# Optimization experiments

Measured on AMD Instinct MI355X. Metric: run time of the kernel, lower is better.

## Reference

```python
import jax, jax.numpy as jnp
import numpy as np

N = 50000      # nodes
E = 800000     # edges
F = 128        # node feature dim (= output_size, residual)
H = 128        # hidden_size

def _uniform_fan_avg(key, shape):
    # VarianceScaling(scale=1.0, mode='fan_avg', distribution='uniform')
    fan_avg = (shape[0] + shape[1]) / 2.0
    limit = np.sqrt(3.0 / fan_avg)
    return jax.random.uniform(key, shape, jnp.float32, -limit, limit)

def setup_inputs() -> dict:
    key = jax.random.key(0)
    ks = jax.random.split(key, 16)
    h = jax.random.normal(ks[0], (N, F), jnp.float32)
    pos = jax.random.normal(ks[1], (N, 3), jnp.float32)
    senders = jax.random.randint(ks[2], (E,), 0, N, jnp.int32)
    receivers = jax.random.randint(ks[3], (E,), 0, N, jnp.int32)
    # edge_mlp: Linear(2F+1 -> H) silu, Linear(H -> H) silu (activate_final=True)
    eW1 = _uniform_fan_avg(ks[4], (2 * F + 1, H)); eb1 = jnp.zeros((H,), jnp.float32)
    eW2 = _uniform_fan_avg(ks[5], (H, H)); eb2 = jnp.zeros((H,), jnp.float32)
    # node_mlp: Linear(F+H -> H) silu, Linear(H -> F) (no final act)
    nW1 = _uniform_fan_avg(ks[6], (F + H, H)); nb1 = jnp.zeros((H,), jnp.float32)
    nW2 = _uniform_fan_avg(ks[7], (H, F)); nb2 = jnp.zeros((F,), jnp.float32)
    # pos_correction_mlp: Linear(H -> H) silu, Linear(H -> 1, no bias, UniformScaling(dt))
    pW1 = _uniform_fan_avg(ks[8], (H, H)); pb1 = jnp.zeros((H,), jnp.float32)
    dt = 0.001
    pW2 = jax.random.uniform(ks[9], (H, 1), jnp.float32, -dt, dt) * np.sqrt(3.0)
    return {"h": h, "pos": pos, "senders": senders, "receivers": receivers,
            "eW1": eW1, "eb1": eb1, "eW2": eW2, "eb2": eb2,
            "nW1": nW1, "nb1": nb1, "nW2": nW2, "nb2": nb2,
            "pW1": pW1, "pb1": pb1, "pW2": pW2}

def reference(h, pos, senders, receivers,
              eW1, eb1, eW2, eb2,
              nW1, nb1, nW2, nb2,
              pW1, pb1, pW2):
    n = h.shape[0]
    # _coord2radial (normalize=False)
    coord_diff = pos[senders] - pos[receivers]            # [E,3]
    radial = jnp.sum(coord_diff ** 2, axis=1, keepdims=True)  # [E,1]
    # edge update (_message): concat(h[senders], h[receivers], radial) -> edge_mlp
    msg_in = jnp.concatenate([h[senders], h[receivers], radial], axis=-1)  # [E,2F+1]
    msg = jax.nn.silu(msg_in @ eW1 + eb1)
    msg = jax.nn.silu(msg @ eW2 + eb2)                    # [E,H]
    # node update (_update): aggregate messages at receivers, node_mlp, residual
    agg = jax.ops.segment_sum(msg, receivers, num_segments=n)  # [N,H]
    x = jnp.concatenate([h, agg], axis=-1)                # [N,F+H]
    x = jax.nn.silu(x @ nW1 + nb1)
    x = x @ nW2 + nb2                                     # [N,F]
    h_new = h + x                                         # residual
    # position update (_pos_update)
    pc = jax.nn.silu(msg @ pW1 + pb1) @ pW2               # [E,1]
    trans = jnp.clip(coord_diff * pc, -100, 100)          # [E,3]
    pos_new = pos + jax.ops.segment_sum(trans, senders, num_segments=n)
    return h_new, pos_new
```

## Files before the change

### kernel.cpp

```cpp
#include <hip/hip_runtime.h>
#include <hip/hip_bf16.h>

#define NNODES 50000
#define NEDGES 800000
#define EB 1024
#define SCAN_BLOCKS 196
#define TRN_BLOCKS 448

typedef short bf16x8 __attribute__((ext_vector_type(8)));
typedef float f32x4 __attribute__((ext_vector_type(4)));
typedef unsigned short u16;
typedef unsigned int u32;

__device__ __forceinline__ u16 f2bf(float f) {
    __hip_bfloat16 b = __float2bfloat16(f);
    return *reinterpret_cast<u16*>(&b);
}
__device__ __forceinline__ float bf2f(u16 v) {
    u32 u = ((u32)v) << 16;
    return __uint_as_float(u);
}
__device__ __forceinline__ u32 pack2(float a, float b) {
    __hip_bfloat162 t = __float22bfloat162_rn(float2{a, b});
    return *reinterpret_cast<u32*>(&t);
}
__device__ __forceinline__ float fast_silu(float x) {
    float e = __builtin_amdgcn_exp2f(-1.442695040888963f * x);
    return x * __builtin_amdgcn_rcpf(1.0f + e);
}
__device__ __forceinline__ bf16x8 ld8(const u16* p) {
    return *(const bf16x8*)p;
}
__device__ __forceinline__ f32x4 mfma16(bf16x8 a, bf16x8 b, f32x4 c) {
    return __builtin_amdgcn_mfma_f32_16x16x32_bf16(a, b, c, 0, 0, 0);
}
__device__ __forceinline__ void bar_lds() {
    asm volatile("s_waitcnt lgkmcnt(0)\n\ts_barrier" ::: "memory");
}

__global__ void prep_kernel(const float* __restrict__ eW1, const float* __restrict__ eW2,
                            const float* __restrict__ pW1, const float* __restrict__ nW1,
                            const float* __restrict__ nW2,
                            u16* __restrict__ eW1T, u16* __restrict__ eW2T,
                            u16* __restrict__ pW1T, u16* __restrict__ nW1T,
                            u16* __restrict__ nW2T,
                            const int* __restrict__ rcv, int* __restrict__ counts) {
    int b = blockIdx.x;
    if (b < TRN_BLOCKS) {
        int i = b * 256 + threadIdx.x;
        const float* src; u16* dst; int K;
        if (i < 32768)      { src = eW1; dst = eW1T; K = 256; }
        else if (i < 49152) { src = eW2; dst = eW2T; K = 128; i -= 32768; }
        else if (i < 65536) { src = pW1; dst = pW1T; K = 128; i -= 49152; }
        else if (i < 98304) { src = nW1; dst = nW1T; K = 256; i -= 65536; }
        else                { src = nW2; dst = nW2T; K = 128; i -= 98304; }
        int n = i / K, k = i - n * K;
        dst[i] = f2bf(src[k * 128 + n]);
    } else {
        int e = (b - TRN_BLOCKS) * 256 + threadIdx.x;
        if (e < NEDGES) atomicAdd(&counts[rcv[e]], 1);
    }
}

__global__ __launch_bounds__(256) void gemm_p(
    const float* __restrict__ h, const u16* __restrict__ eW1T,
    const u16* __restrict__ nW1T, const float* __restrict__ eb1,
    u16* __restrict__ P)
{
    const int tid  = threadIdx.x;
    const int w    = tid >> 6;
    const int lane = tid & 63;
    const int m    = lane & 15;
    const int quad = lane >> 4;
    const int ksub = quad * 8;

    bf16x8 bw[4][6];
    float bias[6];
    #pragma unroll
    for (int cc = 0; cc < 6; cc++) {
        int C = 96 * w + 16 * cc + m;
        const u16* bp;
        if (C < 128)      { bp = eW1T + C * 256;               bias[cc] = 0.5f * eb1[C]; }
        else if (C < 256) { bp = eW1T + (C - 128) * 256 + 128; bias[cc] = 0.5f * eb1[C - 128]; }
        else              { bp = nW1T + (C - 256) * 256;       bias[cc] = 0.f; }
        #pragma unroll
        for (int t = 0; t < 4; t++) bw[t][cc] = ld8(bp + t * 32 + ksub);
    }
    const int base = blockIdx.x * 64;
    #pragma unroll
    for (int mt = 0; mt < 4; mt++) {
        int nm = base + mt * 16 + m;
        if (nm >= NNODES) nm = NNODES - 1;
        bf16x8 afr[4];
        #pragma unroll
        for (int t = 0; t < 4; t++) {
            const float* ap = h + (size_t)nm * 128 + t * 32 + ksub;
            f32x4 lo = *(const f32x4*)ap;
            f32x4 hi = *(const f32x4*)(ap + 4);
            #pragma unroll
            for (int j = 0; j < 4; j++) {
                afr[t][j]     = (short)f2bf(lo[j]);
                afr[t][4 + j] = (short)f2bf(hi[j]);
            }
        }
        f32x4 acc[6];
        #pragma unroll
        for (int cc = 0; cc < 6; cc++) acc[cc] = (f32x4){0,0,0,0};
        #pragma unroll
        for (int t = 0; t < 4; t++)
            #pragma unroll
            for (int cc = 0; cc < 6; cc++)
                acc[cc] = mfma16(afr[t], bw[t][cc], acc[cc]);
        #pragma unroll
        for (int cc = 0; cc < 6; cc++) {
            int C = 96 * w + 16 * cc + m;
            #pragma unroll
            for (int r = 0; r < 4; r++) {
                int nr = base + mt * 16 + quad * 4 + r;
                if (nr < NNODES) P[(size_t)nr * 384 + C] = f2bf(acc[cc][r] + bias[cc]);
            }
        }
    }
}

__global__ void scan1(const int* __restrict__ counts, int* __restrict__ excl,
                      int* __restrict__ blkSum) {
    __shared__ int tmp[256];
    int tx = threadIdx.x;
    int i = blockIdx.x * 256 + tx;
    int v = (i < NNODES) ? counts[i] : 0;
    tmp[tx] = v;
    __syncthreads();
    for (int off = 1; off < 256; off <<= 1) {
        int t = (tx >= off) ? tmp[tx - off] : 0;
        __syncthreads();
        tmp[tx] += t;
        __syncthreads();
    }
    if (i < NNODES) excl[i] = tmp[tx] - v;
    if (tx == 255) blkSum[blockIdx.x] = tmp[255];
}
__global__ void scan2(const int* __restrict__ blkSum, int* __restrict__ blkOff) {
    __shared__ int tmp[256];
    int tx = threadIdx.x;
    int v = (tx < SCAN_BLOCKS) ? blkSum[tx] : 0;
    tmp[tx] = v;
    __syncthreads();
    for (int off = 1; off < 256; off <<= 1) {
        int t = (tx >= off) ? tmp[tx - off] : 0;
        __syncthreads();
        tmp[tx] += t;
        __syncthreads();
    }
    if (tx < SCAN_BLOCKS) blkOff[tx] = tmp[tx] - v;
}
__global__ void scan3(const int* __restrict__ excl, const int* __restrict__ blkOff,
                      int* __restrict__ cursor) {
    int i = blockIdx.x * 256 + threadIdx.x;
    if (i < NNODES) cursor[i] = excl[i] + blkOff[blockIdx.x];
}
__global__ void scatter_kernel(const int* __restrict__ rcv, int* __restrict__ cursor,
                               int* __restrict__ perm) {
    int e = blockIdx.x * 256 + threadIdx.x;
    if (e < NEDGES) {
        int p = atomicAdd(&cursor[rcv[e]], 1);
        perm[p] = e;
    }
}

struct __align__(16) EdgeLds {
    u16   m1[64 * 136];
    u16   msg[64 * 136];
    float diff[64][4];
    float pcpart[4][64];
    float wlast[128];
    int   sndloc[64];
    int   rcvloc[64];
    unsigned long long bmap;
};

__global__ __launch_bounds__(256, 4) void edge_kernel(
    const u16* __restrict__ P, const float* __restrict__ pos,
    const int* __restrict__ snd, const int* __restrict__ rcv,
    const int* __restrict__ perm,
    const float* __restrict__ eW1last,
    const u16* __restrict__ eW2T, const float* __restrict__ eb2,
    const u16* __restrict__ pW1T, const float* __restrict__ pb1,
    const float* __restrict__ pW2,
    float* __restrict__ agg, float* __restrict__ posacc)
{
    __shared__ EdgeLds S;
    const int tid  = threadIdx.x;
    const int w    = tid >> 6;
    const int lane = tid & 63;
    const int m    = lane & 15;
    const int quad = lane >> 4;
    const int ksub = quad * 8;

    bf16x8 bw2[4][2], bp1[4][2];
    float b2v[2], pb1v[2], pw2v[2];
    #pragma unroll
    for (int cc = 0; cc < 2; cc++) {
        int col = (2 * w + cc) * 16 + m;
        #pragma unroll
        for (int t = 0; t < 4; t++) {
            bw2[t][cc] = ld8(eW2T + col * 128 + t * 32 + ksub);
            bp1[t][cc] = ld8(pW1T + col * 128 + t * 32 + ksub);
        }
        b2v[cc]  = eb2[col];
        pb1v[cc] = pb1[col];
        pw2v[cc] = pW2[col];
    }
    if (tid < 128) S.wlast[tid] = eW1last[tid];

    const int NT  = NEDGES / 64;
    const int xcd = blockIdx.x & 7;
    const int ib  = blockIdx.x >> 3;
    const int per = (NT + 7) / 8;
    const int t0  = xcd * per;
    const int t1  = (t0 + per < NT) ? t0 + per : NT;

    int eg_n = 0, s_n = 0, r_n = 0;
    if (t0 + ib < t1) {
        eg_n = perm[(t0 + ib) * 64 + lane];
        s_n = snd[eg_n]; r_n = rcv[eg_n];
    }

    for (int t = t0 + ib; t < t1; t += 128) {
        const int s = s_n, r = r_n;
        const int tn = t + 128;
        const int tp = (tn < t1) ? tn : t;
        int eg2 = perm[tp * 64 + lane];

        float d0 = pos[s * 3 + 0] - pos[r * 3 + 0];
        float d1 = pos[s * 3 + 1] - pos[r * 3 + 1];
        float d2 = pos[s * 3 + 2] - pos[r * 3 + 2];
        float rad = d0 * d0 + d1 * d1 + d2 * d2;

        bar_lds();
        if (tid < 64) {
            S.sndloc[tid] = s; S.rcvloc[tid] = r;
            S.diff[tid][0] = d0; S.diff[tid][1] = d1; S.diff[tid][2] = d2;
            int pv = __shfl_up(r, 1);
            unsigned long long bm = __ballot(lane > 0 && r != pv);
            if (tid == 0) S.bmap = bm;
        }
        {
            const int sw = lane >> 3;
            const u16* pa = P + (size_t)s * 384 + w * 32;
            const u16* pb = P + (size_t)r * 384 + 128 + w * 32;
            #pragma unroll
            for (int k = 0; k < 4; k++) {
                bf16x8 va = ld8(pa + k * 8);
                bf16x8 vb = ld8(pb + k * 8);
                u32 pk[4];
                #pragma unroll
                for (int jj = 0; jj < 4; jj++) {
                    int col = w * 32 + k * 8 + jj * 2;
                    float2 wl = *(const float2*)&S.wlast[col];
                    float v0 = bf2f((u16)va[jj * 2])     + bf2f((u16)vb[jj * 2])     + rad * wl.x;
                    float v1 = bf2f((u16)va[jj * 2 + 1]) + bf2f((u16)vb[jj * 2 + 1]) + rad * wl.y;
                    pk[jj] = pack2(fast_silu(v0), fast_silu(v1));
                }
                int chunk = (w * 4 + k) ^ sw;
                *(uint4*)&S.m1[lane * 136 + chunk * 8] =
                    make_uint4(pk[0], pk[1], pk[2], pk[3]);
            }
        }
        s_n = snd[eg2]; r_n = rcv[eg2]; eg_n = eg2;

        bar_lds();
        #pragma unroll
        for (int mt = 0; mt < 4; mt++) {
            const int rs = mt * 2 + (m >> 3);
            const int row = mt * 16 + m;
            f32x4 acc0 = (f32x4){0,0,0,0}, acc1 = (f32x4){0,0,0,0};
            #pragma unroll
            for (int t4 = 0; t4 < 4; t4++) {
                bf16x8 a = *(const bf16x8*)&S.m1[row * 136 + ((t4 * 4 + quad) ^ rs) * 8];
                acc0 = mfma16(a, bw2[t4][0], acc0);
                acc1 = mfma16(a, bw2[t4][1], acc1);
            }
            #pragma unroll
            for (int cc = 0; cc < 2; cc++) {
                f32x4 acc = cc ? acc1 : acc0;
                int col = (2 * w + cc) * 16 + m;
                #pragma unroll
                for (int rr = 0; rr < 4; rr++) {
                    int orow = mt * 16 + quad * 4 + rr;
                    S.msg[orow * 136 + col] = f2bf(fast_silu(acc[rr] + b2v[cc]));
                }
            }
        }
        bar_lds();
        #pragma unroll
        for (int mt = 0; mt < 4; mt++) {
            f32x4 acc0 = (f32x4){0,0,0,0}, acc1 = (f32x4){0,0,0,0};
            #pragma unroll
            for (int t4 = 0; t4 < 4; t4++) {
                bf16x8 a = *(const bf16x8*)&S.msg[(mt * 16 + m) * 136 + t4 * 32 + ksub];
                acc0 = mfma16(a, bp1[t4][0], acc0);
                acc1 = mfma16(a, bp1[t4][1], acc1);
            }
            float p4[4];
            #pragma unroll
            for (int rr = 0; rr < 4; rr++)
                p4[rr] = fast_silu(acc0[rr] + pb1v[0]) * pw2v[0]
                       + fast_silu(acc1[rr] + pb1v[1]) * pw2v[1];
            #pragma unroll
            for (int mask = 1; mask < 16; mask <<= 1) {
                #pragma unroll
                for (int rr = 0; rr < 4; rr++) p4[rr] += __shfl_xor(p4[rr], mask);
            }
            if (m == 0) {
                #pragma unroll
                for (int rr = 0; rr < 4; rr++)
                    S.pcpart[w][mt * 16 + quad * 4 + rr] = p4[rr];
            }
        }
        {
            int half = tid >> 7, col = tid & 127;
            int r0 = half * 32;
            u32 bm32 = __builtin_amdgcn_readfirstlane((u32)(S.bmap >> r0)) & ~1u;
            float a = 0.f;
            int cur = S.rcvloc[r0];
            int rr = r0;
            const int end0 = r0 + 32;
            while (true) {
                int nb = bm32 ? (r0 + __builtin_ctz(bm32)) : end0;
                for (; rr < nb; ++rr) a += bf2f(S.msg[rr * 136 + col]);
                atomicAdd(&agg[(size_t)cur * 128 + col], a);
                if (nb == end0) break;
                a = 0.f;
                cur = S.rcvloc[nb];
                bm32 &= bm32 - 1;
            }
        }
        bar_lds();
        if (tid < 192) {
            int ee = tid / 3, c = tid - ee * 3;
            float pc = S.pcpart[0][ee] + S.pcpart[1][ee] + S.pcpart[2][ee] + S.pcpart[3][ee];
            float tr = S.diff[ee][c] * pc;
            tr = fminf(fmaxf(tr, -100.f), 100.f);
            atomicAdd(&posacc[S.sndloc[ee] * 3 + c], tr);
        }
    }
}

__global__ __launch_bounds__(256, 4) void node_kernel(
    const u16* __restrict__ P, const float* __restrict__ h,
    const float* __restrict__ agg,
    const u16* __restrict__ nW1T, const float* __restrict__ nb1,
    const u16* __restrict__ nW2T, const float* __restrict__ nb2,
    const float* __restrict__ pos, const float* __restrict__ posacc,
    float* __restrict__ out)
{
    __shared__ alignas(16) u16 m1[64 * 136];
    const int tid  = threadIdx.x;
    const int w    = tid >> 6;
    const int lane = tid & 63;
    const int m    = lane & 15;
    const int quad = lane >> 4;
    const int ksub = quad * 8;

    bf16x8 bw1[4][2], bw2[4][2];
    float b1v[2], b2v[2];
    #pragma unroll
    for (int cc = 0; cc < 2; cc++) {
        int col = (2 * w + cc) * 16 + m;
        #pragma unroll
        for (int t = 0; t < 4; t++) {
            bw1[t][cc] = ld8(nW1T + col * 256 + 128 + t * 32 + ksub);
            bw2[t][cc] = ld8(nW2T + col * 128 + t * 32 + ksub);
        }
        b1v[cc] = nb1[col];
        b2v[cc] = nb2[col];
    }
    const int base = blockIdx.x * 64;
    #pragma unroll
    for (int mt = 0; mt < 4; mt++) {
        int nm = base + mt * 16 + m;
        if (nm >= NNODES) nm = NNODES - 1;
        f32x4 acc0 = (f32x4){0,0,0,0}, acc1 = (f32x4){0,0,0,0};
        #pragma unroll
        for (int t = 0; t < 4; t++) {
            const float* ap = agg + (size_t)nm * 128 + t * 32 + ksub;
            f32x4 lo = *(const f32x4*)ap;
            f32x4 hi = *(const f32x4*)(ap + 4);
            bf16x8 a;
            #pragma unroll
            for (int j = 0; j < 4; j++) {
                a[j]     = (short)f2bf(lo[j]);
                a[4 + j] = (short)f2bf(hi[j]);
            }
            acc0 = mfma16(a, bw1[t][0], acc0);
            acc1 = mfma16(a, bw1[t][1], acc1);
        }
        #pragma unroll
        for (int cc = 0; cc < 2; cc++) {
            f32x4 acc = cc ? acc1 : acc0;
            int col = (2 * w + cc) * 16 + m;
            #pragma unroll
            for (int rr = 0; rr < 4; rr++) {
                int row = mt * 16 + quad * 4 + rr;
                int nrc = base + row; if (nrc >= NNODES) nrc = NNODES - 1;
                float v = acc[rr] + bf2f(P[(size_t)nrc * 384 + 256 + col]) + b1v[cc];
                m1[row * 136 + col] = f2bf(fast_silu(v));
            }
        }
    }
    __syncthreads();
    #pragma unroll
    for (int mt = 0; mt < 4; mt++) {
        f32x4 acc0 = (f32x4){0,0,0,0}, acc1 = (f32x4){0,0,0,0};
        #pragma unroll
        for (int t = 0; t < 4; t++) {
            bf16x8 a = *(const bf16x8*)&m1[(mt * 16 + m) * 136 + t * 32 + ksub];
            acc0 = mfma16(a, bw2[t][0], acc0);
            acc1 = mfma16(a, bw2[t][1], acc1);
        }
        #pragma unroll
        for (int cc = 0; cc < 2; cc++) {
            f32x4 acc = cc ? acc1 : acc0;
            int col = (2 * w + cc) * 16 + m;
            #pragma unroll
            for (int rr = 0; rr < 4; rr++) {
                int nr = base + mt * 16 + quad * 4 + rr;
                if (nr < NNODES)
                    out[(size_t)nr * 128 + col] = acc[rr] + b2v[cc] + h[(size_t)nr * 128 + col];
            }
        }
    }
    if (tid < 192) {
        int i = blockIdx.x * 192 + tid;
        if (i < NNODES * 3) out[NNODES * 128 + i] = pos[i] + posacc[i];
    }
}

extern "C" void kernel_launch(void* const* d_in, const int* in_sizes, int n_in,
                              void* d_out, int out_size, void* d_ws, size_t ws_size,
                              hipStream_t stream) {
    (void)in_sizes; (void)n_in; (void)out_size; (void)ws_size;
    const float* h   = (const float*)d_in[0];
    const float* pos = (const float*)d_in[1];
    const int*   snd = (const int*)d_in[2];
    const int*   rcv = (const int*)d_in[3];
    const float* eW1 = (const float*)d_in[4];
    const float* eb1 = (const float*)d_in[5];
    const float* eW2 = (const float*)d_in[6];
    const float* eb2 = (const float*)d_in[7];
    const float* nW1 = (const float*)d_in[8];
    const float* nb1 = (const float*)d_in[9];
    const float* nW2 = (const float*)d_in[10];
    const float* nb2 = (const float*)d_in[11];
    const float* pW1 = (const float*)d_in[12];
    const float* pb1 = (const float*)d_in[13];
    const float* pW2 = (const float*)d_in[14];
    float* out = (float*)d_out;

    float* agg    = (float*)d_ws;
    float* posacc = agg + (size_t)NNODES * 128;
    u16* P    = (u16*)(posacc + (size_t)NNODES * 3);
    u16* eW1T = P + (size_t)NNODES * 384;
    u16* eW2T = eW1T + 128 * 256;
    u16* pW1T = eW2T + 128 * 128;
    u16* nW1T = pW1T + 128 * 128;
    u16* nW2T = nW1T + 128 * 256;
    int* counts = (int*)(nW2T + 128 * 128);
    int* excl   = counts + 50048;
    int* blkSum = excl + 50048;
    int* blkOff = blkSum + 256;
    int* cursor = blkOff + 256;
    int* perm   = cursor + 50048;

    hipMemsetAsync(agg, 0, (size_t)NNODES * 131 * sizeof(float), stream);
    hipMemsetAsync(counts, 0, 50048 * sizeof(int), stream);

    prep_kernel<<<TRN_BLOCKS + (NEDGES + 255) / 256, 256, 0, stream>>>(
        eW1, eW2, pW1, nW1, nW2, eW1T, eW2T, pW1T, nW1T, nW2T, rcv, counts);

    gemm_p<<<(NNODES + 63) / 64, 256, 0, stream>>>(h, eW1T, nW1T, eb1, P);

    scan1<<<SCAN_BLOCKS, 256, 0, stream>>>(counts, excl, blkSum);
    scan2<<<1, 256, 0, stream>>>(blkSum, blkOff);
    scan3<<<SCAN_BLOCKS, 256, 0, stream>>>(excl, blkOff, cursor);
    scatter_kernel<<<(NEDGES + 255) / 256, 256, 0, stream>>>(rcv, cursor, perm);

    edge_kernel<<<EB, 256, 0, stream>>>(
        P, pos, snd, rcv, perm,
        eW1 + 256 * 128,
        eW2T, eb2, pW1T, pb1, pW2,
        agg, posacc);

    node_kernel<<<(NNODES + 63) / 64, 256, 0, stream>>>(
        P, h, agg, nW1T, nb1, nW2T, nb2, pos, posacc, out);
}
```

Baseline: 454.9 us.

## Prefetch sender rows into LDS asynchronously and fold scan3 into scatter

The edge kernel now uses global_load_lds to stage the next tile's sender projection rows straight into LDS while the current tile's MFMA work runs. It ping-pongs two LDS buffers, so the buffer that held the message tile also receives the prefetch. Separately, the scan3 kernel is dropped: scatter computes each slot as excl+blkOff plus an atomic delta counter, which saves a launch but adds two loads per edge. The risk is a race or mismatched staging layout, since the prefetch into bufM is issued while other waves may still be reading bufM in the pc stage.

```diff
diff --git a/kernel.cpp b/kernel.cpp
--- a/kernel.cpp
+++ b/kernel.cpp
@@ -36,6 +36,11 @@
 }
 __device__ __forceinline__ void bar_lds() {
     asm volatile("s_waitcnt lgkmcnt(0)\n\ts_barrier" ::: "memory");
+}
+__device__ __forceinline__ void stage16(const u16* g, u16* l) {
+    __builtin_amdgcn_global_load_lds(
+        (const __attribute__((address_space(1))) u32*)(const void*)g,
+        (__attribute__((address_space(3))) u32*)(void*)l, 16, 0, 0);
 }
 
 __global__ void prep_kernel(const float* __restrict__ eW1, const float* __restrict__ eW2,
@@ -154,23 +159,20 @@
     }
     if (tx < SCAN_BLOCKS) blkOff[tx] = tmp[tx] - v;
 }
-__global__ void scan3(const int* __restrict__ excl, const int* __restrict__ blkOff,
-                      int* __restrict__ cursor) {
-    int i = blockIdx.x * 256 + threadIdx.x;
-    if (i < NNODES) cursor[i] = excl[i] + blkOff[blockIdx.x];
-}
-__global__ void scatter_kernel(const int* __restrict__ rcv, int* __restrict__ cursor,
+__global__ void scatter_kernel(const int* __restrict__ rcv, const int* __restrict__ excl,
+                               const int* __restrict__ blkOff, int* __restrict__ delta,
                                int* __restrict__ perm) {
     int e = blockIdx.x * 256 + threadIdx.x;
     if (e < NEDGES) {
-        int p = atomicAdd(&cursor[rcv[e]], 1);
+        int r = rcv[e];
+        int p = excl[r] + blkOff[r >> 8] + atomicAdd(&delta[r], 1);
         perm[p] = e;
     }
 }
 
 struct __align__(16) EdgeLds {
-    u16   m1[64 * 136];
-    u16   msg[64 * 136];
+    u16   b0[64 * 136];
+    u16   b1[64 * 136];
     float diff[64][4];
     float pcpart[4][64];
     float wlast[128];
@@ -220,10 +222,16 @@
     const int t0  = xcd * per;
     const int t1  = (t0 + per < NT) ? t0 + per : NT;
 
-    int eg_n = 0, s_n = 0, r_n = 0;
+    u16* bufS = S.b0;
+    u16* bufM = S.b1;
+
+    int s_n = 0, r_n = 0;
     if (t0 + ib < t1) {
-        eg_n = perm[(t0 + ib) * 64 + lane];
-        s_n = snd[eg_n]; r_n = rcv[eg_n];
+        int eg = perm[(t0 + ib) * 64 + lane];
+        s_n = snd[eg]; r_n = rcv[eg];
+        #pragma unroll
+        for (int k = 0; k < 4; k++)
+            stage16(P + (size_t)s_n * 384 + w * 32 + k * 8, bufS + w * 2048 + k * 512);
     }
 
     for (int t = t0 + ib; t < t1; t += 128) {
@@ -247,27 +255,30 @@
         }
         {
             const int sw = lane >> 3;
-            const u16* pa = P + (size_t)s * 384 + w * 32;
-            const u16* pb = P + (size_t)r * 384 + 128 + w * 32;
+            asm volatile("s_waitcnt vmcnt(0)" ::: "memory");
+            bf16x8 va[4];
+            #pragma unroll
+            for (int k = 0; k < 4; k++)
+                va[k] = *(const bf16x8*)&bufS[w * 2048 + k * 512 + lane * 8];
+            const u16* pbp = P + (size_t)r * 384 + 128 + w * 32;
             #pragma unroll
             for (int k = 0; k < 4; k++) {
-                bf16x8 va = ld8(pa + k * 8);
-                bf16x8 vb = ld8(pb + k * 8);
+                bf16x8 vb = ld8(pbp + k * 8);
                 u32 pk[4];
                 #pragma unroll
                 for (int jj = 0; jj < 4; jj++) {
                     int col = w * 32 + k * 8 + jj * 2;
                     float2 wl = *(const float2*)&S.wlast[col];
-                    float v0 = bf2f((u16)va[jj * 2])     + bf2f((u16)vb[jj * 2])     + rad * wl.x;
-                    float v1 = bf2f((u16)va[jj * 2 + 1]) + bf2f((u16)vb[jj * 2 + 1]) + rad * wl.y;
+                    float v0 = bf2f((u16)va[k][jj * 2])     + bf2f((u16)vb[jj * 2])     + rad * wl.x;
+                    float v1 = bf2f((u16)va[k][jj * 2 + 1]) + bf2f((u16)vb[jj * 2 + 1]) + rad * wl.y;
                     pk[jj] = pack2(fast_silu(v0), fast_silu(v1));
                 }
                 int chunk = (w * 4 + k) ^ sw;
-                *(uint4*)&S.m1[lane * 136 + chunk * 8] =
+                *(uint4*)&bufM[lane * 136 + chunk * 8] =
                     make_uint4(pk[0], pk[1], pk[2], pk[3]);
             }
         }
-        s_n = snd[eg2]; r_n = rcv[eg2]; eg_n = eg2;
+        s_n = snd[eg2]; r_n = rcv[eg2];
 
         bar_lds();
         #pragma unroll
@@ -277,7 +288,7 @@
             f32x4 acc0 = (f32x4){0,0,0,0}, acc1 = (f32x4){0,0,0,0};
             #pragma unroll
             for (int t4 = 0; t4 < 4; t4++) {
-                bf16x8 a = *(const bf16x8*)&S.m1[row * 136 + ((t4 * 4 + quad) ^ rs) * 8];
+                bf16x8 a = *(const bf16x8*)&bufM[row * 136 + ((t4 * 4 + quad) ^ rs) * 8];
                 acc0 = mfma16(a, bw2[t4][0], acc0);
                 acc1 = mfma16(a, bw2[t4][1], acc1);
             }
@@ -288,17 +299,21 @@
                 #pragma unroll
                 for (int rr = 0; rr < 4; rr++) {
                     int orow = mt * 16 + quad * 4 + rr;
-                    S.msg[orow * 136 + col] = f2bf(fast_silu(acc[rr] + b2v[cc]));
+                    bufS[orow * 136 + col] = f2bf(fast_silu(acc[rr] + b2v[cc]));
                 }
             }
         }
         bar_lds();
+        #pragma unroll
+        for (int k = 0; k < 4; k++)
+            stage16(P + (size_t)s_n * 384 + w * 32 + k * 8, bufM + w * 2048 + k * 512);
+
         #pragma unroll
         for (int mt = 0; mt < 4; mt++) {
             f32x4 acc0 = (f32x4){0,0,0,0}, acc1 = (f32x4){0,0,0,0};
             #pragma unroll
             for (int t4 = 0; t4 < 4; t4++) {
-                bf16x8 a = *(const bf16x8*)&S.msg[(mt * 16 + m) * 136 + t4 * 32 + ksub];
+                bf16x8 a = *(const bf16x8*)&bufS[(mt * 16 + m) * 136 + t4 * 32 + ksub];
                 acc0 = mfma16(a, bp1[t4][0], acc0);
                 acc1 = mfma16(a, bp1[t4][1], acc1);
             }
@@ -328,7 +343,7 @@
             const int end0 = r0 + 32;
             while (true) {
                 int nb = bm32 ? (r0 + __builtin_ctz(bm32)) : end0;
-                for (; rr < nb; ++rr) a += bf2f(S.msg[rr * 136 + col]);
+                for (; rr < nb; ++rr) a += bf2f(bufS[rr * 136 + col]);
                 atomicAdd(&agg[(size_t)cur * 128 + col], a);
                 if (nb == end0) break;
                 a = 0.f;
@@ -344,6 +359,7 @@
             tr = fminf(fmaxf(tr, -100.f), 100.f);
             atomicAdd(&posacc[S.sndloc[ee] * 3 + c], tr);
         }
+        u16* tmpb = bufS; bufS = bufM; bufM = tmpb;
     }
 }
 
@@ -467,14 +483,14 @@
     u16* nW1T = pW1T + 128 * 128;
     u16* nW2T = nW1T + 128 * 256;
     int* counts = (int*)(nW2T + 128 * 128);
-    int* excl   = counts + 50048;
+    int* delta  = counts + 50048;
+    int* excl   = delta + 50048;
     int* blkSum = excl + 50048;
     int* blkOff = blkSum + 256;
-    int* cursor = blkOff + 256;
-    int* perm   = cursor + 50048;
+    int* perm   = blkOff + 256;
 
     hipMemsetAsync(agg, 0, (size_t)NNODES * 131 * sizeof(float), stream);
-    hipMemsetAsync(counts, 0, 50048 * sizeof(int), stream);
+    hipMemsetAsync(counts, 0, 2 * 50048 * sizeof(int), stream);
 
     prep_kernel<<<TRN_BLOCKS + (NEDGES + 255) / 256, 256, 0, stream>>>(
         eW1, eW2, pW1, nW1, nW2, eW1T, eW2T, pW1T, nW1T, nW2T, rcv, counts);
@@ -483,8 +499,7 @@
 
     scan1<<<SCAN_BLOCKS, 256, 0, stream>>>(counts, excl, blkSum);
     scan2<<<1, 256, 0, stream>>>(blkSum, blkOff);
-    scan3<<<SCAN_BLOCKS, 256, 0, stream>>>(excl, blkOff, cursor);
-    scatter_kernel<<<(NEDGES + 255) / 256, 256, 0, stream>>>(rcv, cursor, perm);
+    scatter_kernel<<<(NEDGES + 255) / 256, 256, 0, stream>>>(rcv, excl, blkOff, delta, perm);
 
     edge_kernel<<<EB, 256, 0, stream>>>(
         P, pos, snd, rcv, perm,
```

New measurement: 504.2 us. +10.8%, slower.

## Precompute sorted sender/receiver pairs and coord diffs during scatter; swizzle msg LDS

Applied to the files above, without the earlier changes.

The scatter kernel now drops the separate scan3 pass and computes each edge's slot directly from excl, blkOff and a per-node atomic delta. It writes sender/receiver pairs and coordinate differences plus the squared radius into receiver-sorted arrays. The edge kernel then reads these contiguously instead of chasing the perm indirection and gathering pos per edge, and it issues the sender-row P loads before the barrier. The msg LDS tile gets an XOR swizzle to avoid bank conflicts, and the segment-sum uses 128 threads each reading two columns at once. The cost is more scatter work and extra workspace for the 24-byte-per-edge arrays.

```diff
diff --git a/kernel.cpp b/kernel.cpp
--- a/kernel.cpp
+++ b/kernel.cpp
@@ -154,17 +154,21 @@
     }
     if (tx < SCAN_BLOCKS) blkOff[tx] = tmp[tx] - v;
 }
-__global__ void scan3(const int* __restrict__ excl, const int* __restrict__ blkOff,
-                      int* __restrict__ cursor) {
-    int i = blockIdx.x * 256 + threadIdx.x;
-    if (i < NNODES) cursor[i] = excl[i] + blkOff[blockIdx.x];
-}
-__global__ void scatter_kernel(const int* __restrict__ rcv, int* __restrict__ cursor,
-                               int* __restrict__ perm) {
+__global__ void scatter_kernel(const int* __restrict__ rcv, const int* __restrict__ snd,
+                               const float* __restrict__ pos,
+                               const int* __restrict__ excl, const int* __restrict__ blkOff,
+                               int* __restrict__ delta,
+                               int2* __restrict__ sr, float4* __restrict__ d4) {
     int e = blockIdx.x * 256 + threadIdx.x;
     if (e < NEDGES) {
-        int p = atomicAdd(&cursor[rcv[e]], 1);
-        perm[p] = e;
+        int r = rcv[e];
+        int s = snd[e];
+        int p = excl[r] + blkOff[r >> 8] + atomicAdd(&delta[r], 1);
+        float d0 = pos[s * 3 + 0] - pos[r * 3 + 0];
+        float d1 = pos[s * 3 + 1] - pos[r * 3 + 1];
+        float d2 = pos[s * 3 + 2] - pos[r * 3 + 2];
+        sr[p] = make_int2(s, r);
+        d4[p] = make_float4(d0, d1, d2, d0 * d0 + d1 * d1 + d2 * d2);
     }
 }
 
@@ -180,9 +184,8 @@
 };
 
 __global__ __launch_bounds__(256, 4) void edge_kernel(
-    const u16* __restrict__ P, const float* __restrict__ pos,
-    const int* __restrict__ snd, const int* __restrict__ rcv,
-    const int* __restrict__ perm,
+    const u16* __restrict__ P,
+    const int2* __restrict__ sr, const float4* __restrict__ d4,
     const float* __restrict__ eW1last,
     const u16* __restrict__ eW2T, const float* __restrict__ eb2,
     const u16* __restrict__ pW1T, const float* __restrict__ pb1,
@@ -220,46 +223,45 @@
     const int t0  = xcd * per;
     const int t1  = (t0 + per < NT) ? t0 + per : NT;
 
-    int eg_n = 0, s_n = 0, r_n = 0;
-    if (t0 + ib < t1) {
-        eg_n = perm[(t0 + ib) * 64 + lane];
-        s_n = snd[eg_n]; r_n = rcv[eg_n];
-    }
+    int2 srn = make_int2(0, 0);
+    if (t0 + ib < t1) srn = sr[(size_t)(t0 + ib) * 64 + lane];
 
     for (int t = t0 + ib; t < t1; t += 128) {
-        const int s = s_n, r = r_n;
+        const int s = srn.x, r = srn.y;
         const int tn = t + 128;
         const int tp = (tn < t1) ? tn : t;
-        int eg2 = perm[tp * 64 + lane];
-
-        float d0 = pos[s * 3 + 0] - pos[r * 3 + 0];
-        float d1 = pos[s * 3 + 1] - pos[r * 3 + 1];
-        float d2 = pos[s * 3 + 2] - pos[r * 3 + 2];
-        float rad = d0 * d0 + d1 * d1 + d2 * d2;
+
+        int2 sr2  = sr[(size_t)tp * 64 + lane];
+        float4 dd = d4[(size_t)t * 64 + lane];
+        const u16* pap = P + (size_t)s * 384 + w * 32;
+        bf16x8 va0 = ld8(pap);
+        bf16x8 va1 = ld8(pap + 8);
+        bf16x8 va2 = ld8(pap + 16);
+        bf16x8 va3 = ld8(pap + 24);
 
         bar_lds();
         if (tid < 64) {
             S.sndloc[tid] = s; S.rcvloc[tid] = r;
-            S.diff[tid][0] = d0; S.diff[tid][1] = d1; S.diff[tid][2] = d2;
+            *(float4*)&S.diff[tid][0] = dd;
             int pv = __shfl_up(r, 1);
             unsigned long long bm = __ballot(lane > 0 && r != pv);
             if (tid == 0) S.bmap = bm;
         }
         {
+            const float rad = dd.w;
             const int sw = lane >> 3;
-            const u16* pa = P + (size_t)s * 384 + w * 32;
-            const u16* pb = P + (size_t)r * 384 + 128 + w * 32;
+            const u16* pbp = P + (size_t)r * 384 + 128 + w * 32;
+            bf16x8 va[4] = {va0, va1, va2, va3};
             #pragma unroll
             for (int k = 0; k < 4; k++) {
-                bf16x8 va = ld8(pa + k * 8);
-                bf16x8 vb = ld8(pb + k * 8);
+                bf16x8 vb = ld8(pbp + k * 8);
                 u32 pk[4];
                 #pragma unroll
                 for (int jj = 0; jj < 4; jj++) {
                     int col = w * 32 + k * 8 + jj * 2;
                     float2 wl = *(const float2*)&S.wlast[col];
-                    float v0 = bf2f((u16)va[jj * 2])     + bf2f((u16)vb[jj * 2])     + rad * wl.x;
-                    float v1 = bf2f((u16)va[jj * 2 + 1]) + bf2f((u16)vb[jj * 2 + 1]) + rad * wl.y;
+                    float v0 = bf2f((u16)va[k][jj * 2])     + bf2f((u16)vb[jj * 2])     + rad * wl.x;
+                    float v1 = bf2f((u16)va[k][jj * 2 + 1]) + bf2f((u16)vb[jj * 2 + 1]) + rad * wl.y;
                     pk[jj] = pack2(fast_silu(v0), fast_silu(v1));
                 }
                 int chunk = (w * 4 + k) ^ sw;
@@ -267,7 +269,7 @@
                     make_uint4(pk[0], pk[1], pk[2], pk[3]);
             }
         }
-        s_n = snd[eg2]; r_n = rcv[eg2]; eg_n = eg2;
+        srn = sr2;
 
         bar_lds();
         #pragma unroll
@@ -285,20 +287,24 @@
             for (int cc = 0; cc < 2; cc++) {
                 f32x4 acc = cc ? acc1 : acc0;
                 int col = (2 * w + cc) * 16 + m;
+                int CC = col >> 3, cl = col & 7;
                 #pragma unroll
                 for (int rr = 0; rr < 4; rr++) {
                     int orow = mt * 16 + quad * 4 + rr;
-                    S.msg[orow * 136 + col] = f2bf(fast_silu(acc[rr] + b2v[cc]));
+                    S.msg[orow * 136 + ((CC ^ (orow >> 3)) << 3) + cl] =
+                        f2bf(fast_silu(acc[rr] + b2v[cc]));
                 }
             }
         }
         bar_lds();
         #pragma unroll
         for (int mt = 0; mt < 4; mt++) {
+            const int row = mt * 16 + m;
+            const int rs = mt * 2 + (m >> 3);
             f32x4 acc0 = (f32x4){0,0,0,0}, acc1 = (f32x4){0,0,0,0};
             #pragma unroll
             for (int t4 = 0; t4 < 4; t4++) {
-                bf16x8 a = *(const bf16x8*)&S.msg[(mt * 16 + m) * 136 + t4 * 32 + ksub];
+                bf16x8 a = *(const bf16x8*)&S.msg[row * 136 + (((t4 * 4 + quad) ^ rs)) * 8];
                 acc0 = mfma16(a, bp1[t4][0], acc0);
                 acc1 = mfma16(a, bp1[t4][1], acc1);
             }
@@ -318,20 +324,28 @@
                     S.pcpart[w][mt * 16 + quad * 4 + rr] = p4[rr];
             }
         }
-        {
-            int half = tid >> 7, col = tid & 127;
+        if (tid < 128) {
+            int half = tid >> 6, cp = tid & 63;
+            int c0 = cp * 2;
             int r0 = half * 32;
             u32 bm32 = __builtin_amdgcn_readfirstlane((u32)(S.bmap >> r0)) & ~1u;
-            float a = 0.f;
+            float a0 = 0.f, a1 = 0.f;
             int cur = S.rcvloc[r0];
             int rr = r0;
             const int end0 = r0 + 32;
+            const int chunkbase = (cp >> 2) ;
+            const int off = (cp & 3) * 2;
             while (true) {
                 int nb = bm32 ? (r0 + __builtin_ctz(bm32)) : end0;
-                for (; rr < nb; ++rr) a += bf2f(S.msg[rr * 136 + col]);
-                atomicAdd(&agg[(size_t)cur * 128 + col], a);
+                for (; rr < nb; ++rr) {
+                    u32 v = *(const u32*)&S.msg[rr * 136 + ((chunkbase ^ (rr >> 3)) << 3) + off];
+                    a0 += bf2f((u16)(v & 0xffff));
+                    a1 += bf2f((u16)(v >> 16));
+                }
+                atomicAdd(&agg[(size_t)cur * 128 + c0], a0);
+                atomicAdd(&agg[(size_t)cur * 128 + c0 + 1], a1);
                 if (nb == end0) break;
-                a = 0.f;
+                a0 = 0.f; a1 = 0.f;
                 cur = S.rcvloc[nb];
                 bm32 &= bm32 - 1;
             }
@@ -467,14 +481,15 @@
     u16* nW1T = pW1T + 128 * 128;
     u16* nW2T = nW1T + 128 * 256;
     int* counts = (int*)(nW2T + 128 * 128);
-    int* excl   = counts + 50048;
+    int* delta  = counts + 50048;
+    int* excl   = delta + 50048;
     int* blkSum = excl + 50048;
     int* blkOff = blkSum + 256;
-    int* cursor = blkOff + 256;
-    int* perm   = cursor + 50048;
+    int2*   sr  = (int2*)(blkOff + 256);
+    float4* d4  = (float4*)(sr + NEDGES);
 
     hipMemsetAsync(agg, 0, (size_t)NNODES * 131 * sizeof(float), stream);
-    hipMemsetAsync(counts, 0, 50048 * sizeof(int), stream);
+    hipMemsetAsync(counts, 0, 2 * 50048 * sizeof(int), stream);
 
     prep_kernel<<<TRN_BLOCKS + (NEDGES + 255) / 256, 256, 0, stream>>>(
         eW1, eW2, pW1, nW1, nW2, eW1T, eW2T, pW1T, nW1T, nW2T, rcv, counts);
@@ -483,11 +498,11 @@
 
     scan1<<<SCAN_BLOCKS, 256, 0, stream>>>(counts, excl, blkSum);
     scan2<<<1, 256, 0, stream>>>(blkSum, blkOff);
-    scan3<<<SCAN_BLOCKS, 256, 0, stream>>>(excl, blkOff, cursor);
-    scatter_kernel<<<(NEDGES + 255) / 256, 256, 0, stream>>>(rcv, cursor, perm);
+    scatter_kernel<<<(NEDGES + 255) / 256, 256, 0, stream>>>(
+        rcv, snd, pos, excl, blkOff, delta, sr, d4);
 
     edge_kernel<<<EB, 256, 0, stream>>>(
-        P, pos, snd, rcv, perm,
+        P, sr, d4,
         eW1 + 256 * 128,
         eW2T, eb2, pW1T, pb1, pW2,
         agg, posacc);
```

Measured after the change: 536.2 us. +17.9%, slower.

## Fold scan3 into scatter, drop edge-kernel barrier, restructure agg segment reduction

Applied to the files above, without the earlier changes.

Removes the scan3 kernel: scatter now computes each slot as the exclusive prefix plus block offset plus an atomic per-node delta. The delta array is zeroed by the same memset as counts. In the edge kernel, each wave's partial position-correction sum now goes straight into the clipped position atomics. This drops the pcpart LDS buffer and the final barrier, but issues four times as many posacc atomics and clips per-wave partial sums instead of the full sum. The message segment reduction now has each wave cover 16 rows with two columns per thread, and the wlast weights are read as vector loads.

```diff
diff --git a/kernel.cpp b/kernel.cpp
--- a/kernel.cpp
+++ b/kernel.cpp
@@ -154,16 +154,13 @@
     }
     if (tx < SCAN_BLOCKS) blkOff[tx] = tmp[tx] - v;
 }
-__global__ void scan3(const int* __restrict__ excl, const int* __restrict__ blkOff,
-                      int* __restrict__ cursor) {
-    int i = blockIdx.x * 256 + threadIdx.x;
-    if (i < NNODES) cursor[i] = excl[i] + blkOff[blockIdx.x];
-}
-__global__ void scatter_kernel(const int* __restrict__ rcv, int* __restrict__ cursor,
+__global__ void scatter_kernel(const int* __restrict__ rcv, const int* __restrict__ excl,
+                               const int* __restrict__ blkOff, int* __restrict__ delta,
                                int* __restrict__ perm) {
     int e = blockIdx.x * 256 + threadIdx.x;
     if (e < NEDGES) {
-        int p = atomicAdd(&cursor[rcv[e]], 1);
+        int r = rcv[e];
+        int p = excl[r] + blkOff[r >> 8] + atomicAdd(&delta[r], 1);
         perm[p] = e;
     }
 }
@@ -172,7 +169,6 @@
     u16   m1[64 * 136];
     u16   msg[64 * 136];
     float diff[64][4];
-    float pcpart[4][64];
     float wlast[128];
     int   sndloc[64];
     int   rcvloc[64];
@@ -240,26 +236,29 @@
         bar_lds();
         if (tid < 64) {
             S.sndloc[tid] = s; S.rcvloc[tid] = r;
-            S.diff[tid][0] = d0; S.diff[tid][1] = d1; S.diff[tid][2] = d2;
+            S.diff[tid][0] = d0; S.diff[tid][1] = d1;
+            S.diff[tid][2] = d2; S.diff[tid][3] = 0.f;
             int pv = __shfl_up(r, 1);
             unsigned long long bm = __ballot(lane > 0 && r != pv);
             if (tid == 0) S.bmap = bm;
         }
         {
             const int sw = lane >> 3;
-            const u16* pa = P + (size_t)s * 384 + w * 32;
-            const u16* pb = P + (size_t)r * 384 + 128 + w * 32;
+            const u16* pap = P + (size_t)s * 384 + w * 32;
+            const u16* pbp = P + (size_t)r * 384 + 128 + w * 32;
             #pragma unroll
             for (int k = 0; k < 4; k++) {
-                bf16x8 va = ld8(pa + k * 8);
-                bf16x8 vb = ld8(pb + k * 8);
+                bf16x8 va = ld8(pap + k * 8);
+                bf16x8 vb = ld8(pbp + k * 8);
+                f32x4 wla = *(const f32x4*)&S.wlast[w * 32 + k * 8];
+                f32x4 wlb = *(const f32x4*)&S.wlast[w * 32 + k * 8 + 4];
                 u32 pk[4];
                 #pragma unroll
                 for (int jj = 0; jj < 4; jj++) {
-                    int col = w * 32 + k * 8 + jj * 2;
-                    float2 wl = *(const float2*)&S.wlast[col];
-                    float v0 = bf2f((u16)va[jj * 2])     + bf2f((u16)vb[jj * 2])     + rad * wl.x;
-                    float v1 = bf2f((u16)va[jj * 2 + 1]) + bf2f((u16)vb[jj * 2 + 1]) + rad * wl.y;
+                    float wx = (jj < 2) ? wla[jj * 2]     : wlb[(jj - 2) * 2];
+                    float wy = (jj < 2) ? wla[jj * 2 + 1] : wlb[(jj - 2) * 2 + 1];
+                    float v0 = bf2f((u16)va[jj * 2])     + bf2f((u16)vb[jj * 2])     + rad * wx;
+                    float v1 = bf2f((u16)va[jj * 2 + 1]) + bf2f((u16)vb[jj * 2 + 1]) + rad * wy;
                     pk[jj] = pack2(fast_silu(v0), fast_silu(v1));
                 }
                 int chunk = (w * 4 + k) ^ sw;
@@ -314,35 +313,43 @@
             }
             if (m == 0) {
                 #pragma unroll
-                for (int rr = 0; rr < 4; rr++)
-                    S.pcpart[w][mt * 16 + quad * 4 + rr] = p4[rr];
+                for (int rr = 0; rr < 4; rr++) {
+                    int row = mt * 16 + quad * 4 + rr;
+                    float pc = p4[rr];
+                    f32x4 dd = *(const f32x4*)&S.diff[row][0];
+                    int sl = S.sndloc[row];
+                    float tr0 = fminf(fmaxf(dd[0] * pc, -100.f), 100.f);
+                    float tr1 = fminf(fmaxf(dd[1] * pc, -100.f), 100.f);
+                    float tr2 = fminf(fmaxf(dd[2] * pc, -100.f), 100.f);
+                    atomicAdd(&posacc[sl * 3 + 0], tr0);
+                    atomicAdd(&posacc[sl * 3 + 1], tr1);
+                    atomicAdd(&posacc[sl * 3 + 2], tr2);
+                }
             }
         }
         {
-            int half = tid >> 7, col = tid & 127;
-            int r0 = half * 32;
-            u32 bm32 = __builtin_amdgcn_readfirstlane((u32)(S.bmap >> r0)) & ~1u;
-            float a = 0.f;
+            int cp = tid & 63;
+            int c0 = cp * 2;
+            int r0 = w * 16;
+            u32 bm = __builtin_amdgcn_readfirstlane(((u32)(S.bmap >> r0)) & 0xFFFFu) & ~1u;
+            float a0 = 0.f, a1 = 0.f;
             int cur = S.rcvloc[r0];
             int rr = r0;
-            const int end0 = r0 + 32;
+            const int end0 = r0 + 16;
             while (true) {
-                int nb = bm32 ? (r0 + __builtin_ctz(bm32)) : end0;
-                for (; rr < nb; ++rr) a += bf2f(S.msg[rr * 136 + col]);
-                atomicAdd(&agg[(size_t)cur * 128 + col], a);
+                int nb = bm ? (r0 + __builtin_ctz(bm)) : end0;
+                for (; rr < nb; ++rr) {
+                    u32 v = *(const u32*)&S.msg[rr * 136 + c0];
+                    a0 += bf2f((u16)(v & 0xffff));
+                    a1 += bf2f((u16)(v >> 16));
+                }
+                atomicAdd(&agg[(size_t)cur * 128 + c0], a0);
+                atomicAdd(&agg[(size_t)cur * 128 + c0 + 1], a1);
                 if (nb == end0) break;
-                a = 0.f;
+                a0 = 0.f; a1 = 0.f;
                 cur = S.rcvloc[nb];
-                bm32 &= bm32 - 1;
-            }
-        }
-        bar_lds();
-        if (tid < 192) {
-            int ee = tid / 3, c = tid - ee * 3;
-            float pc = S.pcpart[0][ee] + S.pcpart[1][ee] + S.pcpart[2][ee] + S.pcpart[3][ee];
-            float tr = S.diff[ee][c] * pc;
-            tr = fminf(fmaxf(tr, -100.f), 100.f);
-            atomicAdd(&posacc[S.sndloc[ee] * 3 + c], tr);
+                bm &= bm - 1;
+            }
         }
     }
 }
@@ -467,14 +474,14 @@
     u16* nW1T = pW1T + 128 * 128;
     u16* nW2T = nW1T + 128 * 256;
     int* counts = (int*)(nW2T + 128 * 128);
-    int* excl   = counts + 50048;
+    int* delta  = counts + 50048;
+    int* excl   = delta + 50048;
     int* blkSum = excl + 50048;
     int* blkOff = blkSum + 256;
-    int* cursor = blkOff + 256;
-    int* perm   = cursor + 50048;
+    int* perm   = blkOff + 256;
 
     hipMemsetAsync(agg, 0, (size_t)NNODES * 131 * sizeof(float), stream);
-    hipMemsetAsync(counts, 0, 50048 * sizeof(int), stream);
+    hipMemsetAsync(counts, 0, 2 * 50048 * sizeof(int), stream);
 
     prep_kernel<<<TRN_BLOCKS + (NEDGES + 255) / 256, 256, 0, stream>>>(
         eW1, eW2, pW1, nW1, nW2, eW1T, eW2T, pW1T, nW1T, nW2T, rcv, counts);
@@ -483,8 +490,8 @@
 
     scan1<<<SCAN_BLOCKS, 256, 0, stream>>>(counts, excl, blkSum);
     scan2<<<1, 256, 0, stream>>>(blkSum, blkOff);
-    scan3<<<SCAN_BLOCKS, 256, 0, stream>>>(excl, blkOff, cursor);
-    scatter_kernel<<<(NEDGES + 255) / 256, 256, 0, stream>>>(rcv, cursor, perm);
+    scatter_kernel<<<(NEDGES + 255) / 256, 256, 0, stream>>>(
+        rcv, excl, blkOff, delta, perm);
 
     edge_kernel<<<EB, 256, 0, stream>>>(
         P, pos, snd, rcv, perm,
```

Measured after the change: 917.0 us. 2.02x slower.
